# Kernel optimization log

Measured on AMD Instinct MI355X. Metric: run time of the kernel, lower is better.

Reference implementation:

```python
import jax, jax.numpy as jnp
import numpy as np

B, S, D, H, F = 2, 2048, 1024, 16, 4096
DH = D // H  # per-head dim = 64
EPS = 1e-5


def _layer_norm(x, g, b):
    mu = jnp.mean(x, axis=-1, keepdims=True)
    var = jnp.mean((x - mu) ** 2, axis=-1, keepdims=True)
    return (x - mu) * jax.lax.rsqrt(var + EPS) * g + b


def _mha(q_in, kv_in, wq, bq, wk, bk, wv, bv, wo, bo, causal):
    b, s, d = q_in.shape
    q = (q_in @ wq + bq).reshape(b, s, H, DH).transpose(0, 2, 1, 3)
    k = (kv_in @ wk + bk).reshape(b, s, H, DH).transpose(0, 2, 1, 3)
    v = (kv_in @ wv + bv).reshape(b, s, H, DH).transpose(0, 2, 1, 3)
    scores = jnp.einsum('bhqd,bhkd->bhqk', q, k) / np.sqrt(DH).astype(np.float32)
    if causal:
        mask = jnp.tril(jnp.ones((s, s), dtype=bool))
        scores = jnp.where(mask, scores, -jnp.inf)
    attn = jax.nn.softmax(scores, axis=-1)
    out = jnp.einsum('bhqk,bhkd->bhqd', attn, v)
    out = out.transpose(0, 2, 1, 3).reshape(b, s, d)
    return out @ wo + bo


def setup_inputs() -> dict:
    key = jax.random.key(0)
    ks = iter(jax.random.split(key, 24))
    def w(shape, fan_in):
        return jax.random.normal(next(ks), shape, jnp.float32) / np.sqrt(fan_in).astype(np.float32)
    inp = {
        'encoder_output': jax.random.normal(next(ks), (B, S, D), jnp.float32),
        'decoder_input': jax.random.normal(next(ks), (B, S, D), jnp.float32),
    }
    for pre in ('sa', 'ca'):
        for nm in ('wq', 'wk', 'wv', 'wo'):
            inp[f'{pre}_{nm}'] = w((D, D), D)
            inp[f'{pre}_b{nm[-1]}'] = jnp.zeros((D,), jnp.float32)
        inp[f'{pre}_g'] = jnp.ones((D,), jnp.float32)
        inp[f'{pre}_bt'] = jnp.zeros((D,), jnp.float32)
    inp['f_w1'] = w((D, F), D); inp['f_b1'] = jnp.zeros((F,), jnp.float32)
    inp['f_w2'] = w((F, D), F); inp['f_b2'] = jnp.zeros((D,), jnp.float32)
    inp['f_g'] = jnp.ones((D,), jnp.float32); inp['f_bt'] = jnp.zeros((D,), jnp.float32)
    return inp


def reference(encoder_output, decoder_input,
              sa_wq, sa_bq, sa_wk, sa_bk, sa_wv, sa_bv, sa_wo, sa_bo, sa_g, sa_bt,
              ca_wq, ca_bq, ca_wk, ca_bk, ca_wv, ca_bv, ca_wo, ca_bo, ca_g, ca_bt,
              f_w1, f_b1, f_w2, f_b2, f_g, f_bt):
    # masked self-attention + residual + LN
    x = _mha(decoder_input, decoder_input, sa_wq, sa_bq, sa_wk, sa_bk, sa_wv, sa_bv, sa_wo, sa_bo, True)
    x = _layer_norm(x + decoder_input, sa_g, sa_bt)
    # encoder-decoder attention + residual + LN
    y = _mha(x, encoder_output, ca_wq, ca_bq, ca_wk, ca_bk, ca_wv, ca_bv, ca_wo, ca_bo, False)
    y = _layer_norm(y + x, ca_g, ca_bt)
    # FFN + residual + LN
    h = jax.nn.relu(y @ f_w1 + f_b1) @ f_w2 + f_b2
    return _layer_norm(h + y, f_g, f_bt)
```

## Files before the change

kernel.cpp:

```cpp
#include <hip/hip_runtime.h>
#include <hip/hip_bf16.h>


typedef __attribute__((ext_vector_type(8))) short bf16x8;
typedef __attribute__((ext_vector_type(4))) float f32x4;
typedef __attribute__((ext_vector_type(16))) float f32x16;

#define LOG2E 1.44269504088896340736f

constexpr int Bb = 2, Ss = 2048, Dd = 1024, Hh = 16, DHd = 64, Ff = 4096;
constexpr int Mrows = Bb * Ss;
constexpr int BHS = Bb * Hh * Ss;

static __device__ __forceinline__ ushort f2b(float f) {
    union { float f; unsigned u; } x{f};
    unsigned r = x.u + 0x7fffu + ((x.u >> 16) & 1u);
    return (ushort)(r >> 16);
}

static __device__ __forceinline__ unsigned pk2(float a, float b) {
    __hip_bfloat162 h = __float22bfloat162_rn(make_float2(a, b));
    unsigned u;
    __builtin_memcpy(&u, &h, 4);
    return u;
}

static __device__ __forceinline__ unsigned pk2t(float a, float b) {
    union { float f; unsigned u; } ua{a}, ub{b};
    return __builtin_amdgcn_perm(ub.u, ua.u, 0x07060302);
}

static __device__ __forceinline__ void gl2lds16(const void* g, void* l) {
    __builtin_amdgcn_global_load_lds(
        (const __attribute__((address_space(1))) void*)g,
        (__attribute__((address_space(3))) void*)l, 16, 0, 0);
}

__global__ __launch_bounds__(256) void cvt_kernel(const float* __restrict__ in,
                                                  ushort* __restrict__ out) {
    int i = (blockIdx.x * 256 + threadIdx.x) * 4;
    float4 v = *(const float4*)(in + i);
    ushort4 u;
    u.x = f2b(v.x); u.y = f2b(v.y); u.z = f2b(v.z); u.w = f2b(v.w);
    *(ushort4*)(out + i) = u;
}

__global__ __launch_bounds__(256) void wtrans_kernel(const float* __restrict__ w,
                                                     ushort* __restrict__ wT,
                                                     int K, int N) {
    __shared__ float t[32][33];
    int tx = threadIdx.x & 31, ty = threadIdx.x >> 5;
    int kb = blockIdx.y * 32, nb = blockIdx.x * 32;
#pragma unroll
    for (int i = 0; i < 4; i++)
        t[ty + i * 8][tx] = w[(size_t)(kb + ty + i * 8) * N + nb + tx];
    __syncthreads();
#pragma unroll
    for (int i = 0; i < 4; i++)
        wT[(size_t)(nb + ty + i * 8) * K + kb + tx] = f2b(t[tx][ty + i * 8]);
}

__global__ __launch_bounds__(256) void pack_bias(const float* __restrict__ a,
                                                 const float* __restrict__ b,
                                                 const float* __restrict__ c,
                                                 float* __restrict__ out) {
    int i = blockIdx.x * 256 + threadIdx.x;
    const float* src = a; int j = i;
    if (i >= 2048)      { src = c; j = i - 2048; }
    else if (i >= 1024) { src = b; j = i - 1024; }
    out[i] = src[j];
}

__global__ __launch_bounds__(256) void gemm_kernel(const ushort* __restrict__ A,
                                                   const ushort* __restrict__ BT,
                                                   const float* __restrict__ bias,
                                                   void* __restrict__ out,
                                                   int M, int N, int K, int klen,
                                                   int mode, int relu, float qsc,
                                                   int vwhich) {
    __shared__ __align__(16) ushort As[128 * 64];
    __shared__ __align__(16) ushort Bs[128 * 64];
    const int tid = threadIdx.x;
    const int lane = tid & 63, wave = tid >> 6;
    const int lr = lane & 15, quad = lane >> 4;
    const int wm = wave & 1, wn = wave >> 1;
    const int m0 = blockIdx.y * 128, n0 = blockIdx.x * 128;
    const int kz = blockIdx.z;
    const int kstart = kz * klen;

    f32x4 acc[4][4];
#pragma unroll
    for (int i = 0; i < 4; i++)
#pragma unroll
        for (int j = 0; j < 4; j++) acc[i][j] = (f32x4){0.f, 0.f, 0.f, 0.f};

    const int srow = tid >> 3;
    const int gchunk = ((tid & 7) ^ (srow & 7)) * 8;
    const ushort* aBase = A + (size_t)(m0 + srow) * K + gchunk;
    const ushort* bBase = BT + (size_t)(n0 + srow) * K + gchunk;
    const size_t rowStep = (size_t)32 * K;

    const int slotA = ((quad) ^ (lr & 7)) * 8;
    const int slotB = ((4 + quad) ^ (lr & 7)) * 8;

    for (int k0 = kstart; k0 < kstart + klen; k0 += 64) {
#pragma unroll
        for (int c = 0; c < 4; c++) {
            gl2lds16(aBase + c * rowStep + k0, &As[c * 2048 + tid * 8]);
            gl2lds16(bBase + c * rowStep + k0, &Bs[c * 2048 + tid * 8]);
        }
        __syncthreads();
#pragma unroll
        for (int kk = 0; kk < 2; kk++) {
            const int slot = kk ? slotB : slotA;
            bf16x8 af[4], bfr[4];
#pragma unroll
            for (int i = 0; i < 4; i++)
                af[i] = *(const bf16x8*)&As[(wm * 64 + i * 16 + lr) * 64 + slot];
#pragma unroll
            for (int j = 0; j < 4; j++)
                bfr[j] = *(const bf16x8*)&Bs[(wn * 64 + j * 16 + lr) * 64 + slot];
#pragma unroll
            for (int i = 0; i < 4; i++)
#pragma unroll
                for (int j = 0; j < 4; j++)
                    acc[i][j] = __builtin_amdgcn_mfma_f32_16x16x32_bf16(af[i], bfr[j], acc[i][j], 0, 0, 0);
        }
        __syncthreads();
    }

#pragma unroll
    for (int j = 0; j < 4; j++) {
        int col = n0 + wn * 64 + j * 16 + lr;
        float bv = (bias && kz == 0) ? bias[col] : 0.f;
#pragma unroll
        for (int i = 0; i < 4; i++) {
            int row0 = m0 + wm * 64 + i * 16 + quad * 4;
            float v[4];
#pragma unroll
            for (int r = 0; r < 4; r++) {
                v[r] = acc[i][j][r] + bv;
                if (relu) v[r] = fmaxf(v[r], 0.f);
            }
            if (mode == 0) {
                float* op = (float*)out + (size_t)kz * M * N;
#pragma unroll
                for (int r = 0; r < 4; r++)
                    op[(size_t)(row0 + r) * N + col] = v[r];
            } else if (mode == 1) {
#pragma unroll
                for (int r = 0; r < 4; r++)
                    ((ushort*)out)[(size_t)(row0 + r) * N + col] = f2b(v[r]);
            } else {
                int which = col >> 10, n1 = col & 1023;
                int h = n1 >> 6, dh = n1 & 63;
                int b = row0 >> 11, s0 = row0 & 2047;
                size_t wbase = (size_t)which * (Bb * Hh * Ss * DHd);
                if (which == vwhich) {
                    uint2 pk;
                    pk.x = pk2(v[0], v[1]); pk.y = pk2(v[2], v[3]);
                    *(uint2*)((ushort*)out + wbase +
                              ((size_t)(b * Hh + h) * DHd + dh) * Ss + s0) = pk;
                } else {
                    float sc = (which == 0) ? qsc : 1.f;
#pragma unroll
                    for (int r = 0; r < 4; r++)
                        ((ushort*)out)[wbase + (((size_t)(b * Hh + h) * Ss + s0 + r) * DHd) + dh] =
                            f2b(v[r] * sc);
                }
            }
        }
    }
}

__global__ __launch_bounds__(256, 2) void attn_kernel(const ushort* __restrict__ Q,
                                                      const ushort* __restrict__ Kg,
                                                      const ushort* __restrict__ VT,
                                                      float* __restrict__ Op0,
                                                      float* __restrict__ Op1,
                                                      float* __restrict__ Ml,
                                                      int causal) {
    __shared__ __align__(16) ushort Ks[64 * 64];
    __shared__ __align__(16) ushort Vs[64 * 64];
    const int tid = threadIdx.x;
    const int lane = tid & 63, w = tid >> 6;
    const int lr31 = lane & 31, hi = lane >> 5, l7 = lane & 7;
    const int hi4 = hi * 4;
    const int p = blockIdx.z;
    const int qt = causal ? (p ? blockIdx.x : (gridDim.x - 1 - blockIdx.x))
                          : blockIdx.x;
    const int bh = blockIdx.y;
    const size_t hb = (size_t)bh * Ss * DHd;
    const int qbase = qt * 256 + w * 64;

    bf16x8 qf[2][4];
#pragma unroll
    for (int qg = 0; qg < 2; qg++)
#pragma unroll
        for (int ks = 0; ks < 4; ks++)
            qf[qg][ks] = *(const bf16x8*)(Q + hb +
                (size_t)(qbase + qg * 32 + lr31) * DHd + ks * 16 + hi * 8);

    f32x16 o[2][2];
#pragma unroll
    for (int i = 0; i < 2; i++)
#pragma unroll
        for (int j = 0; j < 2; j++)
#pragma unroll
            for (int r = 0; r < 16; r++) o[i][j][r] = 0.f;
    float l0 = 0.f, l1 = 0.f;

    const int srow8 = tid >> 3, sslot = tid & 7;
    const int sswz = (sslot ^ (srow8 & 7)) * 8;
    const ushort* kSrc = Kg + hb + (size_t)srow8 * DHd + sswz;
    const ushort* vSrc = VT + hb + (size_t)srow8 * Ss + sswz;

    int so[4];
#pragma unroll
    for (int ks = 0; ks < 4; ks++) so[ks] = ((ks * 2 + hi) ^ l7) * 8;

    const int ktEnd = causal ? (qt + 1) * 4 : (Ss / 64);
    for (int kt = p; kt < ktEnd; kt += 2) {
        const int k0 = kt * 64;
#pragma unroll
        for (int c = 0; c < 2; c++) {
            gl2lds16(kSrc + (size_t)(k0 + c * 32) * DHd, &Ks[c * 2048 + tid * 8]);
            gl2lds16(vSrc + (size_t)(c * 32) * Ss + k0, &Vs[c * 2048 + tid * 8]);
        }
        __syncthreads();
        if (!causal || k0 <= qbase + 63) {
            bf16x8 pb[2][4];
            float ps0 = 0.f, ps1 = 0.f;
            const int maskT = causal && (k0 == qbase);
#pragma unroll
            for (int kg = 0; kg < 2; kg++) {
                bf16x8 kf[4];
#pragma unroll
                for (int ks = 0; ks < 4; ks++)
                    kf[ks] = *(const bf16x8*)&Ks[(kg * 32 + lr31) * 64 + so[ks]];
                f32x16 st[2];
#pragma unroll
                for (int qg = 0; qg < 2; qg++) {
#pragma unroll
                    for (int r = 0; r < 16; r++) st[qg][r] = 0.f;
#pragma unroll
                    for (int ks = 0; ks < 4; ks++)
                        st[qg] = __builtin_amdgcn_mfma_f32_32x32x16_bf16(
                            kf[ks], qf[qg][ks], st[qg], 0, 0, 0);
                }
                if (maskT) {
#pragma unroll
                    for (int r = 0; r < 16; r++) {
                        int klr = kg * 32 + (r & 3) + 8 * (r >> 2) + hi4;
                        st[0][r] = (klr > lr31) ? -1e30f : st[0][r];
                        st[1][r] = (klr > lr31 + 32) ? -1e30f : st[1][r];
                    }
                }
#pragma unroll
                for (int qg = 0; qg < 2; qg++) {
                    float pv[16];
#pragma unroll
                    for (int r = 0; r < 16; r++) {
                        pv[r] = __builtin_amdgcn_exp2f(fminf(st[qg][r], 88.f));
                        if (qg == 0) ps0 += pv[r]; else ps1 += pv[r];
                    }
#pragma unroll
                    for (int t = 0; t < 2; t++) {
                        const int rb = t * 8;
                        unsigned X0 = pk2t(pv[rb + 0], pv[rb + 1]);
                        unsigned X1 = pk2t(pv[rb + 2], pv[rb + 3]);
                        unsigned Y0 = pk2t(pv[rb + 4], pv[rb + 5]);
                        unsigned Y1 = pk2t(pv[rb + 6], pv[rb + 7]);
                        asm("v_permlane32_swap_b32 %0, %1" : "+v"(X0), "+v"(Y0));
                        asm("v_permlane32_swap_b32 %0, %1" : "+v"(X1), "+v"(Y1));
                        union { unsigned u[4]; bf16x8 v; } pw;
                        pw.u[0] = X0; pw.u[1] = X1; pw.u[2] = Y0; pw.u[3] = Y1;
                        pb[qg][kg * 2 + t] = pw.v;
                    }
                }
            }
            l0 += ps0 + __shfl_xor(ps0, 32);
            l1 += ps1 + __shfl_xor(ps1, 32);
#pragma unroll
            for (int ks = 0; ks < 4; ks++) {
                bf16x8 av0 = *(const bf16x8*)&Vs[lr31 * 64 + so[ks]];
                bf16x8 av1 = *(const bf16x8*)&Vs[(32 + lr31) * 64 + so[ks]];
                o[0][0] = __builtin_amdgcn_mfma_f32_32x32x16_bf16(av0, pb[0][ks], o[0][0], 0, 0, 0);
                o[0][1] = __builtin_amdgcn_mfma_f32_32x32x16_bf16(av1, pb[0][ks], o[0][1], 0, 0, 0);
                o[1][0] = __builtin_amdgcn_mfma_f32_32x32x16_bf16(av0, pb[1][ks], o[1][0], 0, 0, 0);
                o[1][1] = __builtin_amdgcn_mfma_f32_32x32x16_bf16(av1, pb[1][ks], o[1][1], 0, 0, 0);
            }
        }
        __syncthreads();
    }

    Ml[(size_t)p * BHS + (size_t)bh * Ss + qbase + lane] = (lane & 32) ? l1 : l0;
    float* Op = p ? Op1 : Op0;
#pragma unroll
    for (int qg = 0; qg < 2; qg++) {
        size_t ob = ((size_t)bh * Ss + qbase + qg * 32 + lr31) * 64;
#pragma unroll
        for (int dhg = 0; dhg < 2; dhg++)
#pragma unroll
            for (int rq = 0; rq < 4; rq++) {
                f32x4 t;
#pragma unroll
                for (int c = 0; c < 4; c++) t[c] = o[qg][dhg][rq * 4 + c];
                *(f32x4*)(Op + ob + dhg * 32 + rq * 8 + hi4) = t;
            }
    }
}

__global__ __launch_bounds__(256) void attn_combine(const float* __restrict__ Op0,
                                                    const float* __restrict__ Op1,
                                                    const float* __restrict__ Ml,
                                                    ushort* __restrict__ O) {
    int g = blockIdx.x * 256 + threadIdx.x;
    int q = g >> 4, seg = g & 15;
    float inv = 1.f / (Ml[q] + Ml[BHS + q]);
    f32x4 x = *(const f32x4*)(Op0 + (size_t)q * 64 + seg * 4);
    f32x4 y = *(const f32x4*)(Op1 + (size_t)q * 64 + seg * 4);
    int bh = q >> 11, sq = q & 2047, bb = bh >> 4, h = bh & 15;
    uint2 u;
    u.x = pk2((x[0] + y[0]) * inv, (x[1] + y[1]) * inv);
    u.y = pk2((x[2] + y[2]) * inv, (x[3] + y[3]) * inv);
    *(uint2*)(O + ((size_t)(bb * Ss + sq)) * Dd + h * 64 + seg * 4) = u;
}

__global__ __launch_bounds__(256) void ln_kernel(const float* __restrict__ a0,
                                                 const float* __restrict__ a1,
                                                 const float* __restrict__ a2,
                                                 const float* __restrict__ a3,
                                                 const float* __restrict__ resid,
                                                 const float* __restrict__ g,
                                                 const float* __restrict__ bt,
                                                 float* __restrict__ out32,
                                                 ushort* __restrict__ outb) {
    const int row = blockIdx.x, tid = threadIdx.x;
    const size_t base = (size_t)row * Dd + tid * 4;
    float4 av = *(const float4*)(a0 + base);
    if (a1) { float4 t = *(const float4*)(a1 + base); av.x += t.x; av.y += t.y; av.z += t.z; av.w += t.w; }
    if (a2) { float4 t = *(const float4*)(a2 + base); av.x += t.x; av.y += t.y; av.z += t.z; av.w += t.w; }
    if (a3) { float4 t = *(const float4*)(a3 + base); av.x += t.x; av.y += t.y; av.z += t.z; av.w += t.w; }
    float4 rv = *(const float4*)(resid + base);
    float x0 = av.x + rv.x, x1 = av.y + rv.y, x2 = av.z + rv.z, x3 = av.w + rv.w;
    float s = x0 + x1 + x2 + x3;
    float q = x0 * x0 + x1 * x1 + x2 * x2 + x3 * x3;
#pragma unroll
    for (int off = 1; off <= 32; off <<= 1) {
        s += __shfl_xor(s, off);
        q += __shfl_xor(q, off);
    }
    __shared__ float red[8];
    int wave = tid >> 6, lane = tid & 63;
    if (lane == 0) { red[wave] = s; red[4 + wave] = q; }
    __syncthreads();
    s = red[0] + red[1] + red[2] + red[3];
    q = red[4] + red[5] + red[6] + red[7];
    float mu = s * (1.f / Dd);
    float var = q * (1.f / Dd) - mu * mu;
    float rs = rsqrtf(var + 1e-5f);
    int col = tid * 4;
    float4 gv = *(const float4*)(g + col);
    float4 bv = *(const float4*)(bt + col);
    float y0 = (x0 - mu) * rs * gv.x + bv.x;
    float y1 = (x1 - mu) * rs * gv.y + bv.y;
    float y2 = (x2 - mu) * rs * gv.z + bv.z;
    float y3 = (x3 - mu) * rs * gv.w + bv.w;
    if (out32) *(float4*)(out32 + base) = make_float4(y0, y1, y2, y3);
    if (outb) {
        ushort4 u; u.x = f2b(y0); u.y = f2b(y1); u.z = f2b(y2); u.w = f2b(y3);
        *(ushort4*)(outb + base) = u;
    }
}

constexpr size_t OFF_XB     = 0;
constexpr size_t OFF_ENCB   = OFF_XB     + 8388608;
constexpr size_t OFF_QKVWT  = OFF_ENCB   + 8388608;
constexpr size_t OFF_CAWQT  = OFF_QKVWT  + 6291456;
constexpr size_t OFF_CAKVT  = OFF_CAWQT  + 2097152;
constexpr size_t OFF_SAWOT  = OFF_CAKVT  + 4194304;
constexpr size_t OFF_CAWOT  = OFF_SAWOT  + 2097152;
constexpr size_t OFF_FW1T   = OFF_CAWOT  + 2097152;
constexpr size_t OFF_FW2T   = OFF_FW1T   + 8388608;
constexpr size_t OFF_SABQKV = OFF_FW2T   + 8388608;
constexpr size_t OFF_CABKV  = OFF_SABQKV + 12288;
constexpr size_t OFF_QB     = OFF_CABKV  + 8192;
constexpr size_t OFF_KB     = OFF_QB     + 8388608;
constexpr size_t OFF_VB     = OFF_KB     + 8388608;
constexpr size_t OFF_ATTNO  = OFF_VB     + 8388608;
constexpr size_t OFF_F1     = OFF_ATTNO  + 8388608;
constexpr size_t OFF_F2     = OFF_F1     + 16777216;
constexpr size_t OFF_X1B    = OFF_F2     + 16777216;
constexpr size_t OFF_F3     = OFF_X1B    + 8388608;
constexpr size_t OFF_YB     = OFF_F3     + 16777216;
constexpr size_t OFF_H1B    = OFF_YB     + 8388608;

extern "C" void kernel_launch(void* const* d_in, const int* in_sizes, int n_in,
                              void* d_out, int out_size, void* d_ws, size_t ws_size,
                              hipStream_t stream) {
    const float* enc   = (const float*)d_in[0];
    const float* dec   = (const float*)d_in[1];
    const float* sa_wq = (const float*)d_in[2];
    const float* sa_bq = (const float*)d_in[3];
    const float* sa_wk = (const float*)d_in[4];
    const float* sa_bk = (const float*)d_in[5];
    const float* sa_wv = (const float*)d_in[6];
    const float* sa_bv = (const float*)d_in[7];
    const float* sa_wo = (const float*)d_in[8];
    const float* sa_bo = (const float*)d_in[9];
    const float* sa_g  = (const float*)d_in[10];
    const float* sa_bt = (const float*)d_in[11];
    const float* ca_wq = (const float*)d_in[12];
    const float* ca_bq = (const float*)d_in[13];
    const float* ca_wk = (const float*)d_in[14];
    const float* ca_bk = (const float*)d_in[15];
    const float* ca_wv = (const float*)d_in[16];
    const float* ca_bv = (const float*)d_in[17];
    const float* ca_wo = (const float*)d_in[18];
    const float* ca_bo = (const float*)d_in[19];
    const float* ca_g  = (const float*)d_in[20];
    const float* ca_bt = (const float*)d_in[21];
    const float* f_w1  = (const float*)d_in[22];
    const float* f_b1  = (const float*)d_in[23];
    const float* f_w2  = (const float*)d_in[24];
    const float* f_b2  = (const float*)d_in[25];
    const float* f_g   = (const float*)d_in[26];
    const float* f_bt  = (const float*)d_in[27];

    char* ws = (char*)d_ws;
    ushort* xb     = (ushort*)(ws + OFF_XB);
    ushort* encb   = (ushort*)(ws + OFF_ENCB);
    ushort* qkvwT  = (ushort*)(ws + OFF_QKVWT);
    ushort* cawqT  = (ushort*)(ws + OFF_CAWQT);
    ushort* cakvT  = (ushort*)(ws + OFF_CAKVT);
    ushort* sawoT  = (ushort*)(ws + OFF_SAWOT);
    ushort* cawoT  = (ushort*)(ws + OFF_CAWOT);
    ushort* fw1T   = (ushort*)(ws + OFF_FW1T);
    ushort* fw2T   = (ushort*)(ws + OFF_FW2T);
    float*  sabqkv = (float*)(ws + OFF_SABQKV);
    float*  cabkv  = (float*)(ws + OFF_CABKV);
    ushort* qb     = (ushort*)(ws + OFF_QB);
    ushort* kb     = (ushort*)(ws + OFF_KB);
    ushort* vbt    = (ushort*)(ws + OFF_VB);
    ushort* attno  = (ushort*)(ws + OFF_ATTNO);
    float*  f1     = (float*)(ws + OFF_F1);
    float*  f2     = (float*)(ws + OFF_F2);
    ushort* x1b    = (ushort*)(ws + OFF_X1B);
    float*  x1f    = (float*)(ws + OFF_F3);
    ushort* yb     = (ushort*)(ws + OFF_YB);
    ushort* h1b    = (ushort*)(ws + OFF_H1B);
    float*  yfp    = (float*)(ws + OFF_QB);
    float*  ml     = (float*)(ws + OFF_H1B);

    const float QSC = 0.125f * LOG2E;
    const size_t MN = (size_t)Mrows * Dd;

    cvt_kernel<<<4096, 256, 0, stream>>>(dec, xb);
    cvt_kernel<<<4096, 256, 0, stream>>>(enc, encb);
    dim3 tgDD(32, 32);
    wtrans_kernel<<<tgDD, 256, 0, stream>>>(sa_wq, qkvwT,                 Dd, Dd);
    wtrans_kernel<<<tgDD, 256, 0, stream>>>(sa_wk, qkvwT + 1024 * 1024,   Dd, Dd);
    wtrans_kernel<<<tgDD, 256, 0, stream>>>(sa_wv, qkvwT + 2 * 1024 * 1024, Dd, Dd);
    wtrans_kernel<<<tgDD, 256, 0, stream>>>(sa_wo, sawoT,                 Dd, Dd);
    wtrans_kernel<<<tgDD, 256, 0, stream>>>(ca_wq, cawqT,                 Dd, Dd);
    wtrans_kernel<<<tgDD, 256, 0, stream>>>(ca_wk, cakvT,                 Dd, Dd);
    wtrans_kernel<<<tgDD, 256, 0, stream>>>(ca_wv, cakvT + 1024 * 1024,   Dd, Dd);
    wtrans_kernel<<<tgDD, 256, 0, stream>>>(ca_wo, cawoT,                 Dd, Dd);
    wtrans_kernel<<<dim3(128, 32), 256, 0, stream>>>(f_w1, fw1T, Dd, Ff);
    wtrans_kernel<<<dim3(32, 128), 256, 0, stream>>>(f_w2, fw2T, Ff, Dd);
    pack_bias<<<12, 256, 0, stream>>>(sa_bq, sa_bk, sa_bv, sabqkv);
    pack_bias<<<8, 256, 0, stream>>>(ca_bk, ca_bv, nullptr, cabkv);

    gemm_kernel<<<dim3(24, 32, 1), 256, 0, stream>>>(xb, qkvwT, sabqkv, qb,
                                                     Mrows, 3072, Dd, Dd, 2, 0, QSC, 2);
    attn_kernel<<<dim3(8, 32, 2), 256, 0, stream>>>(qb, kb, vbt, f1, x1f, ml, 1);
    attn_combine<<<4096, 256, 0, stream>>>(f1, x1f, ml, attno);
    gemm_kernel<<<dim3(8, 32, 2), 256, 0, stream>>>(attno, sawoT, sa_bo, f1,
                                                    Mrows, Dd, Dd, 512, 0, 0, 1.f, -1);
    ln_kernel<<<4096, 256, 0, stream>>>(f1, f2, nullptr, nullptr, dec,
                                        sa_g, sa_bt, x1f, x1b);

    gemm_kernel<<<dim3(8, 32, 1), 256, 0, stream>>>(x1b, cawqT, ca_bq, qb,
                                                    Mrows, Dd, Dd, Dd, 2, 0, QSC, -1);
    gemm_kernel<<<dim3(16, 32, 1), 256, 0, stream>>>(encb, cakvT, cabkv, kb,
                                                     Mrows, 2048, Dd, Dd, 2, 0, 1.f, 1);
    attn_kernel<<<dim3(8, 32, 2), 256, 0, stream>>>(qb, kb, vbt, f1, f2, ml, 0);
    attn_combine<<<4096, 256, 0, stream>>>(f1, f2, ml, attno);
    gemm_kernel<<<dim3(8, 32, 2), 256, 0, stream>>>(attno, cawoT, ca_bo, f1,
                                                    Mrows, Dd, Dd, 512, 0, 0, 1.f, -1);
    ln_kernel<<<4096, 256, 0, stream>>>(f1, f2, nullptr, nullptr, x1f,
                                        ca_g, ca_bt, yfp, yb);

    gemm_kernel<<<dim3(32, 32, 1), 256, 0, stream>>>(yb, fw1T, f_b1, h1b,
                                                     Mrows, Ff, Dd, Dd, 1, 1, 1.f, -1);
    gemm_kernel<<<dim3(8, 32, 4), 256, 0, stream>>>(h1b, fw2T, f_b2, f1,
                                                    Mrows, Dd, Ff, 1024, 0, 0, 1.f, -1);
    ln_kernel<<<4096, 256, 0, stream>>>(f1, f1 + MN, f1 + 2 * MN, f1 + 3 * MN, yfp,
                                        f_g, f_bt, (float*)d_out, nullptr);
}
```

Baseline: 576.4 us.

## Add 256x256 double-buffered GEMM with XCD-aware block remapping for large projections

Adds a new 512-thread GEMM kernel with 256x256 output tiles, double-buffered LDS and an explicitly phased schedule. Global-to-LDS prefetches for the next K tile are interleaved with MFMA phases, and s_setprio raises wave priority during the MFMA bursts. Both GEMM kernels remap block indices so that consecutive blocks are spread across the 8 XCDs. The large QKV, cross-attention KV and FFN GEMMs switch to the new kernel to get more data reuse per tile and to overlap loads with compute. In exchange the grids are smaller (for example 192 blocks for QKV), which may leave CUs idle, and the manual waitcnt and barrier choreography is fragile.

```diff
diff --git a/kernel.cpp b/kernel.cpp
--- a/kernel.cpp
+++ b/kernel.cpp
@@ -84,7 +84,10 @@
     const int lane = tid & 63, wave = tid >> 6;
     const int lr = lane & 15, quad = lane >> 4;
     const int wm = wave & 1, wn = wave >> 1;
-    const int m0 = blockIdx.y * 128, n0 = blockIdx.x * 128;
+    const int nwg = gridDim.x * gridDim.y;
+    const int orig = blockIdx.y * gridDim.x + blockIdx.x;
+    const int wg = (orig & 7) * (nwg >> 3) + (orig >> 3);
+    const int m0 = (wg / gridDim.x) * 128, n0 = (wg % gridDim.x) * 128;
     const int kz = blockIdx.z;
     const int kstart = kz * klen;
 
@@ -136,6 +139,165 @@
 #pragma unroll
         for (int i = 0; i < 4; i++) {
             int row0 = m0 + wm * 64 + i * 16 + quad * 4;
+            float v[4];
+#pragma unroll
+            for (int r = 0; r < 4; r++) {
+                v[r] = acc[i][j][r] + bv;
+                if (relu) v[r] = fmaxf(v[r], 0.f);
+            }
+            if (mode == 0) {
+                float* op = (float*)out + (size_t)kz * M * N;
+#pragma unroll
+                for (int r = 0; r < 4; r++)
+                    op[(size_t)(row0 + r) * N + col] = v[r];
+            } else if (mode == 1) {
+#pragma unroll
+                for (int r = 0; r < 4; r++)
+                    ((ushort*)out)[(size_t)(row0 + r) * N + col] = f2b(v[r]);
+            } else {
+                int which = col >> 10, n1 = col & 1023;
+                int h = n1 >> 6, dh = n1 & 63;
+                int b = row0 >> 11, s0 = row0 & 2047;
+                size_t wbase = (size_t)which * (Bb * Hh * Ss * DHd);
+                if (which == vwhich) {
+                    uint2 pk;
+                    pk.x = pk2(v[0], v[1]); pk.y = pk2(v[2], v[3]);
+                    *(uint2*)((ushort*)out + wbase +
+                              ((size_t)(b * Hh + h) * DHd + dh) * Ss + s0) = pk;
+                } else {
+                    float sc = (which == 0) ? qsc : 1.f;
+#pragma unroll
+                    for (int r = 0; r < 4; r++)
+                        ((ushort*)out)[wbase + (((size_t)(b * Hh + h) * Ss + s0 + r) * DHd) + dh] =
+                            f2b(v[r] * sc);
+                }
+            }
+        }
+    }
+}
+
+#define MFMAP(I0)                                                              \
+    __builtin_amdgcn_s_setprio(1);                                             \
+    _Pragma("unroll")                                                          \
+    for (int j = 0; j < 4; j++) {                                              \
+        acc[I0][j] = __builtin_amdgcn_mfma_f32_16x16x32_bf16(af[0][0], bfr[j][0], acc[I0][j], 0, 0, 0);         \
+        acc[I0][j] = __builtin_amdgcn_mfma_f32_16x16x32_bf16(af[0][1], bfr[j][1], acc[I0][j], 0, 0, 0);         \
+        acc[I0 + 1][j] = __builtin_amdgcn_mfma_f32_16x16x32_bf16(af[1][0], bfr[j][0], acc[I0 + 1][j], 0, 0, 0); \
+        acc[I0 + 1][j] = __builtin_amdgcn_mfma_f32_16x16x32_bf16(af[1][1], bfr[j][1], acc[I0 + 1][j], 0, 0, 0); \
+    }                                                                          \
+    __builtin_amdgcn_s_setprio(0);
+
+#define PHASE_READ_A(IB)                                                       \
+    af[0][0] = *(const bf16x8*)&Ac[aoff0 + (IB) * 1024];                       \
+    af[0][1] = *(const bf16x8*)&Ac[aoff1 + (IB) * 1024];                       \
+    af[1][0] = *(const bf16x8*)&Ac[aoff0 + ((IB) + 1) * 1024];                 \
+    af[1][1] = *(const bf16x8*)&Ac[aoff1 + ((IB) + 1) * 1024];
+
+#define GTILE(PF)                                                              \
+  {                                                                            \
+    const ushort* Ac = &As[(t & 1) * 16384];                                   \
+    const ushort* Bc = &Bs[(t & 1) * 16384];                                   \
+    const int nb = (t & 1) ^ 1;                                                \
+    const int kn = kstart + (t + 1) * 64;                                      \
+    bf16x8 bfr[4][2], af[2][2];                                                \
+                                                        \
+    _Pragma("unroll")                                                          \
+    for (int j = 0; j < 4; j++) {                                              \
+        bfr[j][0] = *(const bf16x8*)&Bc[boff0 + j * 1024];                     \
+        bfr[j][1] = *(const bf16x8*)&Bc[boff1 + j * 1024];                     \
+    }                                                                          \
+    PHASE_READ_A(0)                                                            \
+    if (PF) { stB(nb, kn, 0); stB(nb, kn, 1); }                                \
+    __builtin_amdgcn_s_barrier();                                              \
+    asm volatile("s_waitcnt lgkmcnt(0)" ::: "memory");                         \
+    MFMAP(0)                                                                   \
+    __builtin_amdgcn_s_barrier();                                              \
+                                                        \
+    PHASE_READ_A(2)                                                            \
+    if (PF) { stB(nb, kn, 2); stB(nb, kn, 3); }                                \
+    __builtin_amdgcn_s_barrier();                                              \
+    asm volatile("s_waitcnt lgkmcnt(0)" ::: "memory");                         \
+    MFMAP(2)                                                                   \
+    if (PF) asm volatile("s_waitcnt vmcnt(4)" ::: "memory");                   \
+    else    asm volatile("s_waitcnt vmcnt(0)" ::: "memory");                   \
+    __builtin_amdgcn_s_barrier();                                              \
+                                                        \
+    PHASE_READ_A(4)                                                            \
+    if (PF) { stA(nb, kn, 0); stA(nb, kn, 2); }                                \
+    __builtin_amdgcn_s_barrier();                                              \
+    asm volatile("s_waitcnt lgkmcnt(0)" ::: "memory");                         \
+    MFMAP(4)                                                                   \
+    __builtin_amdgcn_s_barrier();                                              \
+                                                        \
+    PHASE_READ_A(6)                                                            \
+    if (PF) { stA(nb, kn, 1); stA(nb, kn, 3); }                                \
+    __builtin_amdgcn_s_barrier();                                              \
+    asm volatile("s_waitcnt lgkmcnt(0)" ::: "memory");                         \
+    MFMAP(6)                                                                   \
+    if (PF) asm volatile("s_waitcnt vmcnt(2)" ::: "memory");                   \
+    __builtin_amdgcn_s_barrier();                                              \
+  }
+
+__global__ __launch_bounds__(512) void gemm256(const ushort* __restrict__ A,
+                                               const ushort* __restrict__ BT,
+                                               const float* __restrict__ bias,
+                                               void* __restrict__ out,
+                                               int M, int N, int K, int klen,
+                                               int mode, int relu, float qsc,
+                                               int vwhich) {
+    __shared__ __align__(16) ushort As[2 * 16384];
+    __shared__ __align__(16) ushort Bs[2 * 16384];
+    const int tid = threadIdx.x;
+    const int lane = tid & 63, wave = tid >> 6;
+    const int lr = lane & 15, quad = lane >> 4;
+    const int wm = wave & 1, wn = wave >> 1;
+    const int nwg = gridDim.x * gridDim.y;
+    const int orig = blockIdx.y * gridDim.x + blockIdx.x;
+    const int wg = (orig & 7) * (nwg >> 3) + (orig >> 3);
+    const int m0 = (wg / gridDim.x) * 256, n0 = (wg % gridDim.x) * 256;
+    const int kz = blockIdx.z;
+    const int kstart = kz * klen;
+
+    f32x4 acc[8][4];
+#pragma unroll
+    for (int i = 0; i < 8; i++)
+#pragma unroll
+        for (int j = 0; j < 4; j++) acc[i][j] = (f32x4){0.f, 0.f, 0.f, 0.f};
+
+    const int srow = tid >> 3;
+    const int gchunk = ((tid & 7) ^ (srow & 7)) * 8;
+    const ushort* aBase = A + (size_t)(m0 + srow) * K + gchunk;
+    const ushort* bBase = BT + (size_t)(n0 + srow) * K + gchunk;
+    const size_t rowStep = (size_t)64 * K;
+
+    auto stA = [&](int b, int kn, int c) {
+        gl2lds16(aBase + (size_t)c * rowStep + kn, &As[b * 16384 + c * 4096 + tid * 8]);
+    };
+    auto stB = [&](int b, int kn, int c) {
+        gl2lds16(bBase + (size_t)c * rowStep + kn, &Bs[b * 16384 + c * 4096 + tid * 8]);
+    };
+
+    const int aoff0 = (wm * 128 + lr) * 64 + (((0 * 4 + quad)) ^ (lr & 7)) * 8;
+    const int aoff1 = (wm * 128 + lr) * 64 + (((1 * 4 + quad)) ^ (lr & 7)) * 8;
+    const int boff0 = (wn * 64 + lr) * 64 + (((0 * 4 + quad)) ^ (lr & 7)) * 8;
+    const int boff1 = (wn * 64 + lr) * 64 + (((1 * 4 + quad)) ^ (lr & 7)) * 8;
+
+    stB(0, kstart, 0); stB(0, kstart, 1); stB(0, kstart, 2); stB(0, kstart, 3);
+    stA(0, kstart, 0); stA(0, kstart, 2); stA(0, kstart, 1); stA(0, kstart, 3);
+    asm volatile("s_waitcnt vmcnt(2)" ::: "memory");
+    __builtin_amdgcn_s_barrier();
+
+    const int nkt = klen >> 6;
+    for (int t = 0; t < nkt - 1; t++) GTILE(1)
+    { const int t = nkt - 1; GTILE(0) }
+
+#pragma unroll
+    for (int j = 0; j < 4; j++) {
+        int col = n0 + wn * 64 + j * 16 + lr;
+        float bv = (bias && kz == 0) ? bias[col] : 0.f;
+#pragma unroll
+        for (int i = 0; i < 8; i++) {
+            int row0 = m0 + wm * 128 + i * 16 + quad * 4;
             float v[4];
 #pragma unroll
             for (int r = 0; r < 4; r++) {
@@ -265,8 +427,8 @@
                         if (qg == 0) ps0 += pv[r]; else ps1 += pv[r];
                     }
 #pragma unroll
-                    for (int t = 0; t < 2; t++) {
-                        const int rb = t * 8;
+                    for (int tt = 0; tt < 2; tt++) {
+                        const int rb = tt * 8;
                         unsigned X0 = pk2t(pv[rb + 0], pv[rb + 1]);
                         unsigned X1 = pk2t(pv[rb + 2], pv[rb + 3]);
                         unsigned Y0 = pk2t(pv[rb + 4], pv[rb + 5]);
@@ -275,7 +437,7 @@
                         asm("v_permlane32_swap_b32 %0, %1" : "+v"(X1), "+v"(Y1));
                         union { unsigned u[4]; bf16x8 v; } pw;
                         pw.u[0] = X0; pw.u[1] = X1; pw.u[2] = Y0; pw.u[3] = Y1;
-                        pb[qg][kg * 2 + t] = pw.v;
+                        pb[qg][kg * 2 + tt] = pw.v;
                     }
                 }
             }
@@ -472,8 +634,8 @@
     pack_bias<<<12, 256, 0, stream>>>(sa_bq, sa_bk, sa_bv, sabqkv);
     pack_bias<<<8, 256, 0, stream>>>(ca_bk, ca_bv, nullptr, cabkv);
 
-    gemm_kernel<<<dim3(24, 32, 1), 256, 0, stream>>>(xb, qkvwT, sabqkv, qb,
-                                                     Mrows, 3072, Dd, Dd, 2, 0, QSC, 2);
+    gemm256<<<dim3(12, 16, 1), 512, 0, stream>>>(xb, qkvwT, sabqkv, qb,
+                                                 Mrows, 3072, Dd, Dd, 2, 0, QSC, 2);
     attn_kernel<<<dim3(8, 32, 2), 256, 0, stream>>>(qb, kb, vbt, f1, x1f, ml, 1);
     attn_combine<<<4096, 256, 0, stream>>>(f1, x1f, ml, attno);
     gemm_kernel<<<dim3(8, 32, 2), 256, 0, stream>>>(attno, sawoT, sa_bo, f1,
@@ -483,8 +645,8 @@
 
     gemm_kernel<<<dim3(8, 32, 1), 256, 0, stream>>>(x1b, cawqT, ca_bq, qb,
                                                     Mrows, Dd, Dd, Dd, 2, 0, QSC, -1);
-    gemm_kernel<<<dim3(16, 32, 1), 256, 0, stream>>>(encb, cakvT, cabkv, kb,
-                                                     Mrows, 2048, Dd, Dd, 2, 0, 1.f, 1);
+    gemm256<<<dim3(8, 16, 1), 512, 0, stream>>>(encb, cakvT, cabkv, kb,
+                                                Mrows, 2048, Dd, Dd, 2, 0, 1.f, 1);
     attn_kernel<<<dim3(8, 32, 2), 256, 0, stream>>>(qb, kb, vbt, f1, f2, ml, 0);
     attn_combine<<<4096, 256, 0, stream>>>(f1, f2, ml, attno);
     gemm_kernel<<<dim3(8, 32, 2), 256, 0, stream>>>(attno, cawoT, ca_bo, f1,
@@ -492,10 +654,10 @@
     ln_kernel<<<4096, 256, 0, stream>>>(f1, f2, nullptr, nullptr, x1f,
                                         ca_g, ca_bt, yfp, yb);
 
-    gemm_kernel<<<dim3(32, 32, 1), 256, 0, stream>>>(yb, fw1T, f_b1, h1b,
-                                                     Mrows, Ff, Dd, Dd, 1, 1, 1.f, -1);
-    gemm_kernel<<<dim3(8, 32, 4), 256, 0, stream>>>(h1b, fw2T, f_b2, f1,
-                                                    Mrows, Dd, Ff, 1024, 0, 0, 1.f, -1);
+    gemm256<<<dim3(16, 16, 1), 512, 0, stream>>>(yb, fw1T, f_b1, h1b,
+                                                 Mrows, Ff, Dd, Dd, 1, 1, 1.f, -1);
+    gemm256<<<dim3(4, 16, 4), 512, 0, stream>>>(h1b, fw2T, f_b2, f1,
+                                                Mrows, Dd, Ff, 1024, 0, 0, 1.f, -1);
     ln_kernel<<<4096, 256, 0, stream>>>(f1, f1 + MN, f1 + 2 * MN, f1 + 3 * MN, yfp,
                                         f_g, f_bt, (float*)d_out, nullptr);
 }
```

Result: no change. 566.5 us (-1.7%).
